# Performance work log

Hardware: AMD Instinct MI355X
Metric: run time of the kernel (lower is better)

The kernel has to match this reference:

```python
import jax, jax.numpy as jnp
import numpy as np

KERNEL_SIZES = (3, 5, 7)
NUM_HEAD = 6
DIM = 192
K_SCALES = 3
HEADS_PER_SCALE = NUM_HEAD // K_SCALES  # 2
HEAD_DIM = DIM // NUM_HEAD              # 32
SCALE = HEAD_DIM ** -0.5


def _nbr_idx(L, K):
    # NATTEN non-causal, dilation=1: window centered on query, clamped at edges.
    start = jnp.clip(jnp.arange(L) - K // 2, 0, L - K)
    return start[:, None] + jnp.arange(K)  # [L, K]


def _na3d_branch(xi, K):
    # xi: [B, D, H, W, C] with C = 3 * HEADS_PER_SCALE * HEAD_DIM
    B, D, H, W, C = xi.shape
    qkv = xi.reshape(B, D, H, W, 3, HEADS_PER_SCALE, HEAD_DIM).transpose(4, 0, 5, 1, 2, 3, 6)
    q, k, v = qkv[0] * SCALE, qkv[1], qkv[2]  # each [B, h, D, H, W, hd]

    idd, idh, idw = _nbr_idx(D, K), _nbr_idx(H, K), _nbr_idx(W, K)

    def gather(t):
        t = jnp.take(t, idd, axis=2)  # [B,h,D,K,H,W,hd]
        t = jnp.take(t, idh, axis=4)  # [B,h,D,K,H,K,W,hd]
        t = jnp.take(t, idw, axis=6)  # [B,h,D,K,H,K,W,K,hd]
        return t

    kn = gather(k)
    vn = gather(v)
    # attention logits over the K^3 neighborhood per query
    attn = jnp.einsum('bndhwc,bndihjwkc->bndhwijk', q, kn)
    attn = jax.nn.softmax(attn.reshape(B, HEADS_PER_SCALE, D, H, W, K ** 3), axis=-1)
    attn = attn.reshape(B, HEADS_PER_SCALE, D, H, W, K, K, K)
    y = jnp.einsum('bndhwijk,bndihjwkc->bndhwc', attn, vn)
    # [B,h,D,H,W,hd] -> [B,D,H,W,h*hd]
    return y.transpose(0, 2, 3, 4, 1, 5).reshape(B, D, H, W, HEADS_PER_SCALE * HEAD_DIM)


def setup_inputs() -> dict:
    key = jax.random.key(0)
    k0, k1, k2 = jax.random.split(key, 3)
    x = jax.random.normal(k0, (1, 8, 24, 24, DIM), dtype=jnp.float32)
    W_qkv = jax.random.normal(k1, (DIM, 3 * DIM), dtype=jnp.float32) * 0.02
    b_qkv = jnp.zeros((3 * DIM,), dtype=jnp.float32)
    W_proj = jax.random.normal(k2, (DIM, DIM), dtype=jnp.float32) * 0.02
    b_proj = jnp.zeros((DIM,), dtype=jnp.float32)
    return {'x': x, 'W_qkv': W_qkv, 'b_qkv': b_qkv, 'W_proj': W_proj, 'b_proj': b_proj}


def reference(x, W_qkv, b_qkv, W_proj, b_proj):
    qkv = x @ W_qkv + b_qkv  # [B,D,H,W,3*DIM]
    # torch.split with channels [DIM, DIM, DIM]
    chunks = jnp.split(qkv, K_SCALES, axis=4)
    ys = [_na3d_branch(chunks[i], KERNEL_SIZES[i]) for i in range(K_SCALES)]
    y = jnp.concatenate(ys, axis=4)  # [B,D,H,W,DIM]
    return y @ W_proj + b_proj
```

## Files before the change

### kernel.cpp

```cpp
#include <hip/hip_runtime.h>

typedef unsigned short ushort_t;
typedef unsigned int uint_t;
typedef __attribute__((ext_vector_type(8))) _Float16 half8;
typedef __attribute__((ext_vector_type(4))) float f32x4;

constexpr int DD = 8, HH = 24, WW = 24;
constexpr int NQ = DD * HH * WW;
constexpr int CIN = 192;
constexpr int CQKV = 576;
constexpr int KW = 192;
constexpr float SCALE_LOG2E = 0.17677669529663687f * 1.4426950408889634f;
constexpr int NROW = DD * HH;

__device__ __forceinline__ ushort_t bf16h(float x) {
    uint_t u = __float_as_uint(x);
    u += 0x7FFFu + ((u >> 16) & 1u);
    return (ushort_t)(u >> 16);
}
__device__ __forceinline__ float2 unpack2(uint_t u) {
    return make_float2(__uint_as_float(u << 16),
                       __uint_as_float(u & 0xffff0000u));
}
__device__ __forceinline__ ushort_t f16h(float x) {
    _Float16 h = (_Float16)x;
    return __builtin_bit_cast(ushort_t, h);
}
__device__ __forceinline__ float f16f(ushort_t h) {
    return (float)__builtin_bit_cast(_Float16, h);
}
__device__ __forceinline__ float quad_add_xor1(float x) {
    return x + __int_as_float(__builtin_amdgcn_mov_dpp(__float_as_int(x), 0xB1, 0xF, 0xF, true));
}
__device__ __forceinline__ float quad_add_xor2(float x) {
    return x + __int_as_float(__builtin_amdgcn_mov_dpp(__float_as_int(x), 0x4E, 0xF, 0xF, true));
}

constexpr int EB0 = 0;
constexpr int EB1 = NROW * 2 * WW * 2;
constexpr int EB2 = EB1 + NROW * 3 * WW * 2;
constexpr int ETOT = EB2 + NROW * 4 * WW * 2;

__global__ __launch_bounds__(256)
void convert_w_kernel(const float* __restrict__ Wq, const float* __restrict__ Wp,
                      ushort_t* __restrict__ Bq, ushort_t* __restrict__ Bp)
{
    __shared__ float T[32][36];
    int b = blockIdx.x;
    const float* W; ushort_t* Bb; int N;
    int kt, nt;
    if (b < 108) { W = Wq; Bb = Bq; N = CQKV; kt = b % 6; nt = b / 6; }
    else         { b -= 108; W = Wp; Bb = Bp; N = CIN; kt = b % 6; nt = b / 6; }
    const int k0 = kt * 32, n0 = nt * 32;
    const int tid = threadIdx.x;

    #pragma unroll
    for (int p = 0; p < 4; ++p) {
        int e = p * 256 + tid;
        int r = e >> 5, c = e & 31;
        T[c][r] = W[(long)(k0 + r) * N + n0 + c];
    }
    __syncthreads();
    const int n = tid >> 3;
    const int k4 = (tid & 7) * 4;
    float4 v = *(const float4*)(&T[n][k4]);
    ushort4 hv;
    hv.x = f16h(v.x); hv.y = f16h(v.y); hv.z = f16h(v.z); hv.w = f16h(v.w);
    *(ushort4*)(Bb + (long)(n0 + n) * KW + k0 + k4) = hv;
}

__global__ __launch_bounds__(256)
void gemm_mfma_kernel(const float* __restrict__ A, const ushort_t* __restrict__ Bb,
                      const float* __restrict__ bias, ushort_t* __restrict__ Cout, int N)
{
    __shared__ ushort_t As[64][72];
    __shared__ ushort_t Bs[64][72];
    __shared__ float Ct[64][68];

    const int tid = threadIdx.x;
    const int bm = blockIdx.x * 64;
    const int bn = blockIdx.y * 64;

    const int wv = tid >> 6;
    const int lane = tid & 63;
    const int lm = lane & 15;
    const int quad = lane >> 4;
    const int wr = (wv >> 1) * 32;
    const int wc = (wv & 1) * 32;

    const int ar = tid >> 4;
    const int ac4 = (tid & 15) * 4;
    const int br0 = tid >> 3;
    const int bc0 = (tid & 7) * 8;

    f32x4 acc[2][2] = {};

    float4 av[4];
    #pragma unroll
    for (int p = 0; p < 4; ++p)
        av[p] = *(const float4*)(A + (long)(bm + ar + p * 16) * CIN + ac4);
    uint4 nb0 = *(const uint4*)(Bb + (long)(bn + br0) * KW + bc0);
    uint4 nb1 = *(const uint4*)(Bb + (long)(bn + br0 + 32) * KW + bc0);

    #pragma unroll
    for (int g = 0; g < 3; ++g) {
        const uint4 b0 = nb0, b1 = nb1;
        ushort4 hv4[4], lv4[4];
        #pragma unroll
        for (int p = 0; p < 4; ++p) {
            float4 v = av[p];
            hv4[p].x = f16h(v.x); hv4[p].y = f16h(v.y);
            hv4[p].z = f16h(v.z); hv4[p].w = f16h(v.w);
            lv4[p].x = f16h(v.x - f16f(hv4[p].x));
            lv4[p].y = f16h(v.y - f16f(hv4[p].y));
            lv4[p].z = f16h(v.z - f16f(hv4[p].z));
            lv4[p].w = f16h(v.w - f16f(hv4[p].w));
        }
        __syncthreads();
        #pragma unroll
        for (int p = 0; p < 4; ++p)
            *(ushort4*)(&As[ar + p * 16][ac4]) = hv4[p];
        *(uint4*)(&Bs[br0][bc0])      = b0;
        *(uint4*)(&Bs[br0 + 32][bc0]) = b1;
        if (g < 2) {
            const int kk = (g + 1) * 64;
            nb0 = *(const uint4*)(Bb + (long)(bn + br0) * KW + kk + bc0);
            nb1 = *(const uint4*)(Bb + (long)(bn + br0 + 32) * KW + kk + bc0);
            #pragma unroll
            for (int p = 0; p < 4; ++p)
                av[p] = *(const float4*)(A + (long)(bm + ar + p * 16) * CIN + (g + 1) * 64 + ac4);
        }
        __syncthreads();

        #pragma unroll
        for (int ks = 0; ks < 64; ks += 32) {
            half8 af0 = *(const half8*)(&As[wr + lm][ks + quad * 8]);
            half8 af1 = *(const half8*)(&As[wr + 16 + lm][ks + quad * 8]);
            half8 bf0 = *(const half8*)(&Bs[wc + lm][ks + quad * 8]);
            half8 bf1 = *(const half8*)(&Bs[wc + 16 + lm][ks + quad * 8]);
            acc[0][0] = __builtin_amdgcn_mfma_f32_16x16x32_f16(af0, bf0, acc[0][0], 0, 0, 0);
            acc[0][1] = __builtin_amdgcn_mfma_f32_16x16x32_f16(af0, bf1, acc[0][1], 0, 0, 0);
            acc[1][0] = __builtin_amdgcn_mfma_f32_16x16x32_f16(af1, bf0, acc[1][0], 0, 0, 0);
            acc[1][1] = __builtin_amdgcn_mfma_f32_16x16x32_f16(af1, bf1, acc[1][1], 0, 0, 0);
        }
        __syncthreads();
        #pragma unroll
        for (int p = 0; p < 4; ++p)
            *(ushort4*)(&As[ar + p * 16][ac4]) = lv4[p];
        __syncthreads();
        #pragma unroll
        for (int ks = 0; ks < 64; ks += 32) {
            half8 af0 = *(const half8*)(&As[wr + lm][ks + quad * 8]);
            half8 af1 = *(const half8*)(&As[wr + 16 + lm][ks + quad * 8]);
            half8 bf0 = *(const half8*)(&Bs[wc + lm][ks + quad * 8]);
            half8 bf1 = *(const half8*)(&Bs[wc + 16 + lm][ks + quad * 8]);
            acc[0][0] = __builtin_amdgcn_mfma_f32_16x16x32_f16(af0, bf0, acc[0][0], 0, 0, 0);
            acc[0][1] = __builtin_amdgcn_mfma_f32_16x16x32_f16(af0, bf1, acc[0][1], 0, 0, 0);
            acc[1][0] = __builtin_amdgcn_mfma_f32_16x16x32_f16(af1, bf0, acc[1][0], 0, 0, 0);
            acc[1][1] = __builtin_amdgcn_mfma_f32_16x16x32_f16(af1, bf1, acc[1][1], 0, 0, 0);
        }
    }

    #pragma unroll
    for (int tc = 0; tc < 2; ++tc) {
        const float bv = bias[bn + wc + tc * 16 + lm];
        #pragma unroll
        for (int tr = 0; tr < 2; ++tr) {
            #pragma unroll
            for (int reg = 0; reg < 4; ++reg)
                Ct[wr + tr * 16 + quad * 4 + reg][wc + tc * 16 + lm] = acc[tr][tc][reg] + bv;
        }
    }
    __syncthreads();
    const int orow = tid >> 4;
    const int oc4 = (tid & 15) * 4;
    #pragma unroll
    for (int p = 0; p < 4; ++p) {
        const int r = orow + p * 16;
        float4 v = *(const float4*)(&Ct[r][oc4]);
        ushort4 hv;
        hv.x = bf16h(v.x); hv.y = bf16h(v.y); hv.z = bf16h(v.z); hv.w = bf16h(v.w);
        *(ushort4*)(Cout + (long)(bm + r) * N + bn + oc4) = hv;
    }
}

__global__ __launch_bounds__(256)
void gemm_proj_kernel(const float* __restrict__ accs, const float* __restrict__ stats,
                      const ushort_t* __restrict__ Bb, const float* __restrict__ bias,
                      float* __restrict__ Cout)
{
    __shared__ ushort_t As[64][72];
    __shared__ ushort_t Bs[64][72];
    __shared__ float Ct[64][68];

    const int tid = threadIdx.x;
    const int bm = blockIdx.x * 64;
    const int bn = blockIdx.y * 64;

    const int wv = tid >> 6;
    const int lane = tid & 63;
    const int lm = lane & 15;
    const int quad = lane >> 4;
    const int wr = (wv >> 1) * 32;
    const int wc = (wv & 1) * 32;

    const int ar = tid >> 4;
    const int ac4 = (tid & 15) * 4;
    const int a_hd = ac4 >> 5;
    const int a_cc = ac4 & 31;
    const int br0 = tid >> 3;
    const int bc0 = (tid & 7) * 8;

    f32x4 acc[2][2] = {};

    auto load_av = [&](int gg, float4* av) {
        const int CK = gg + 2;
        const int eb = (gg == 0) ? EB0 : (gg == 1 ? EB1 : EB2);
        #pragma unroll
        for (int p = 0; p < 4; ++p) {
            const int q = bm + ar + p * 16;
            const int rr = q / WW;
            const int w = q - rr * WW;
            const int e0 = eb + (rr * CK) * (WW * 2) + w * 2 + a_hd;
            float S = 0.f;
            float4 a = make_float4(0.f, 0.f, 0.f, 0.f);
            #pragma unroll
            for (int c = 0; c < 4; ++c) {
                if (c < CK) {
                    const int e = e0 + c * (WW * 2);
                    S += stats[e];
                    const float4 t = *(const float4*)(accs + (long)e * 32 + a_cc);
                    a.x += t.x; a.y += t.y; a.z += t.z; a.w += t.w;
                }
            }
            const float rs = 1.0f / S;
            av[p] = make_float4(a.x * rs, a.y * rs, a.z * rs, a.w * rs);
        }
    };

    float4 av[4];
    load_av(0, av);
    uint4 nb0 = *(const uint4*)(Bb + (long)(bn + br0) * KW + bc0);
    uint4 nb1 = *(const uint4*)(Bb + (long)(bn + br0 + 32) * KW + bc0);

    #pragma unroll
    for (int g = 0; g < 3; ++g) {
        const uint4 b0 = nb0, b1 = nb1;
        ushort4 hv4[4], lv4[4];
        #pragma unroll
        for (int p = 0; p < 4; ++p) {
            float4 v = av[p];
            hv4[p].x = f16h(v.x); hv4[p].y = f16h(v.y);
            hv4[p].z = f16h(v.z); hv4[p].w = f16h(v.w);
            lv4[p].x = f16h(v.x - f16f(hv4[p].x));
            lv4[p].y = f16h(v.y - f16f(hv4[p].y));
            lv4[p].z = f16h(v.z - f16f(hv4[p].z));
            lv4[p].w = f16h(v.w - f16f(hv4[p].w));
        }
        __syncthreads();
        #pragma unroll
        for (int p = 0; p < 4; ++p)
            *(ushort4*)(&As[ar + p * 16][ac4]) = hv4[p];
        *(uint4*)(&Bs[br0][bc0])      = b0;
        *(uint4*)(&Bs[br0 + 32][bc0]) = b1;
        if (g < 2) {
            const int kk = (g + 1) * 64;
            nb0 = *(const uint4*)(Bb + (long)(bn + br0) * KW + kk + bc0);
            nb1 = *(const uint4*)(Bb + (long)(bn + br0 + 32) * KW + kk + bc0);
            load_av(g + 1, av);
        }
        __syncthreads();

        #pragma unroll
        for (int ks = 0; ks < 64; ks += 32) {
            half8 af0 = *(const half8*)(&As[wr + lm][ks + quad * 8]);
            half8 af1 = *(const half8*)(&As[wr + 16 + lm][ks + quad * 8]);
            half8 bf0 = *(const half8*)(&Bs[wc + lm][ks + quad * 8]);
            half8 bf1 = *(const half8*)(&Bs[wc + 16 + lm][ks + quad * 8]);
            acc[0][0] = __builtin_amdgcn_mfma_f32_16x16x32_f16(af0, bf0, acc[0][0], 0, 0, 0);
            acc[0][1] = __builtin_amdgcn_mfma_f32_16x16x32_f16(af0, bf1, acc[0][1], 0, 0, 0);
            acc[1][0] = __builtin_amdgcn_mfma_f32_16x16x32_f16(af1, bf0, acc[1][0], 0, 0, 0);
            acc[1][1] = __builtin_amdgcn_mfma_f32_16x16x32_f16(af1, bf1, acc[1][1], 0, 0, 0);
        }
        __syncthreads();
        #pragma unroll
        for (int p = 0; p < 4; ++p)
            *(ushort4*)(&As[ar + p * 16][ac4]) = lv4[p];
        __syncthreads();
        #pragma unroll
        for (int ks = 0; ks < 64; ks += 32) {
            half8 af0 = *(const half8*)(&As[wr + lm][ks + quad * 8]);
            half8 af1 = *(const half8*)(&As[wr + 16 + lm][ks + quad * 8]);
            half8 bf0 = *(const half8*)(&Bs[wc + lm][ks + quad * 8]);
            half8 bf1 = *(const half8*)(&Bs[wc + 16 + lm][ks + quad * 8]);
            acc[0][0] = __builtin_amdgcn_mfma_f32_16x16x32_f16(af0, bf0, acc[0][0], 0, 0, 0);
            acc[0][1] = __builtin_amdgcn_mfma_f32_16x16x32_f16(af0, bf1, acc[0][1], 0, 0, 0);
            acc[1][0] = __builtin_amdgcn_mfma_f32_16x16x32_f16(af1, bf0, acc[1][0], 0, 0, 0);
            acc[1][1] = __builtin_amdgcn_mfma_f32_16x16x32_f16(af1, bf1, acc[1][1], 0, 0, 0);
        }
    }

    #pragma unroll
    for (int tc = 0; tc < 2; ++tc) {
        const float bv = bias[bn + wc + tc * 16 + lm];
        #pragma unroll
        for (int tr = 0; tr < 2; ++tr) {
            #pragma unroll
            for (int reg = 0; reg < 4; ++reg)
                Ct[wr + tr * 16 + quad * 4 + reg][wc + tc * 16 + lm] = acc[tr][tc][reg] + bv;
        }
    }
    __syncthreads();
    const int orow = tid >> 4;
    const int oc4 = (tid & 15) * 4;
    #pragma unroll
    for (int p = 0; p < 4; ++p) {
        const int r = orow + p * 16;
        float4 v = *(const float4*)(&Ct[r][oc4]);
        *(float4*)(Cout + (long)(bm + r) * CIN + bn + oc4) = v;
    }
}

constexpr int KROW = 72;
constexpr int RBUF = WW * KROW;

template<int K>
__device__ __forceinline__
void split_chunk(const ushort_t* __restrict__ qkv,
                 float* __restrict__ accs, float* __restrict__ stats,
                 int r, int c, int nchunks, int scale, int ebase,
                 int w, int hd, int d8, int tid,
                 ushort_t* __restrict__ ksh, ushort_t* __restrict__ vsh)
{
    const int i0 = 2 * c;
    const int ni = (K - i0) < 2 ? (K - i0) : 2;
    const int NT = ni * K;

    const int dq = r / HH, hq = r % HH;
    int sd = dq - K / 2; sd = sd < 0 ? 0 : (sd > DD - K ? DD - K : sd);
    int sh = hq - K / 2; sh = sh < 0 ? 0 : (sh > HH - K ? HH - K : sh);
    int sw = w  - K / 2; sw = sw < 0 ? 0 : (sw > WW - K ? WW - K : sw);

    const int q = (dq * HH + hq) * WW + w;

    uint4 qu = *(const uint4*)(qkv + (long)q * CQKV + scale * 192 + hd * 32 + d8 * 8);
    float2 qf[4] = {unpack2(qu.x), unpack2(qu.y), unpack2(qu.z), unpack2(qu.w)};
    #pragma unroll
    for (int t = 0; t < 4; ++t) {
        qf[t].x *= SCALE_LOG2E;
        qf[t].y *= SCALE_LOG2E;
    }

    const int lw = tid >> 3;
    const int c8 = (tid & 7) * 8;

    auto src_ptr = [&](int t) {
        int i = i0 + t / K;
        int j = t - (t / K) * K;
        return qkv + (long)(((sd + i) * HH + (sh + j)) * WW + lw) * CQKV
             + scale * 192 + c8;
    };

    uint4 ck, cv;
    {
        const ushort_t* p0 = src_ptr(0);
        uint4 k0 = *(const uint4*)(p0 + 64);
        uint4 v0 = *(const uint4*)(p0 + 128);
        const ushort_t* p1 = src_ptr(1);
        ck = *(const uint4*)(p1 + 64);
        cv = *(const uint4*)(p1 + 128);
        *(uint4*)(ksh + lw * KROW + c8) = k0;
        *(uint4*)(vsh + lw * KROW + c8) = v0;
    }

    float sum = 0.f;
    float2 acc[4] = {};
    const int choff = hd * 32 + d8 * 8;

    for (int t = 0; t < NT; ++t) {
        __syncthreads();
        uint4 nk, nv;
        const bool issue = (t + 2 < NT);
        if (issue) {
            const ushort_t* pn = src_ptr(t + 2);
            nk = *(const uint4*)(pn + 64);
            nv = *(const uint4*)(pn + 128);
        }

        const ushort_t* kb = ksh + (t % 3) * RBUF + choff;
        const ushort_t* vb = vsh + (t % 3) * RBUF + choff;
        #pragma unroll
        for (int n = 0; n < K; ++n) {
            uint4 ku = *(const uint4*)(kb + (sw + n) * KROW);
            float2 k0 = unpack2(ku.x), k1 = unpack2(ku.y),
                   k2 = unpack2(ku.z), k3 = unpack2(ku.w);
            float2 d;
            d.x  = qf[0].x * k0.x; d.y  = qf[0].y * k0.y;
            d.x += qf[1].x * k1.x; d.y += qf[1].y * k1.y;
            d.x += qf[2].x * k2.x; d.y += qf[2].y * k2.y;
            d.x += qf[3].x * k3.x; d.y += qf[3].y * k3.y;
            float p = d.x + d.y;
            p = quad_add_xor1(p);
            p = quad_add_xor2(p);
            float pr = exp2f(p);
            sum += pr;
            uint4 vu = *(const uint4*)(vb + (sw + n) * KROW);
            float2 v0 = unpack2(vu.x), v1 = unpack2(vu.y),
                   v2 = unpack2(vu.z), v3 = unpack2(vu.w);
            acc[0].x += pr * v0.x; acc[0].y += pr * v0.y;
            acc[1].x += pr * v1.x; acc[1].y += pr * v1.y;
            acc[2].x += pr * v2.x; acc[2].y += pr * v2.y;
            acc[3].x += pr * v3.x; acc[3].y += pr * v3.y;
        }

        if (t + 1 < NT) {
            *(uint4*)(ksh + ((t + 1) % 3) * RBUF + lw * KROW + c8) = ck;
            *(uint4*)(vsh + ((t + 1) % 3) * RBUF + lw * KROW + c8) = cv;
        }
        ck = nk; cv = nv;
    }

    const int e = ebase + ((r * nchunks + c) * WW + w) * 2 + hd;
    if (d8 == 0) stats[e] = sum;
    float* ap = accs + (long)e * 32 + d8 * 8;
    *(float4*)(ap)     = make_float4(acc[0].x, acc[0].y, acc[1].x, acc[1].y);
    *(float4*)(ap + 4) = make_float4(acc[2].x, acc[2].y, acc[3].x, acc[3].y);
}

__global__ __launch_bounds__(192)
void na3d_split_kernel(const ushort_t* __restrict__ qkv,
                       float* __restrict__ accs, float* __restrict__ stats)
{
    __shared__ alignas(16) ushort_t ksh[3 * RBUF];
    __shared__ alignas(16) ushort_t vsh[3 * RBUF];

    const int tid = threadIdx.x;
    const int w  = tid >> 3;
    const int hd = (tid >> 2) & 1;
    const int d8 = tid & 3;

    const int orig = blockIdx.x;
    int bid;
    if (orig < NROW * 4) {
        bid = (orig & 7) * (NROW * 4 / 8) + (orig >> 3);
    } else if (orig < NROW * 7) {
        const int t = orig - NROW * 4;
        bid = NROW * 4 + (t & 7) * (NROW * 3 / 8) + (t >> 3);
    } else {
        const int t = orig - NROW * 7;
        bid = NROW * 7 + (t & 7) * (NROW * 2 / 8) + (t >> 3);
    }

    if (bid < NROW * 4) {
        int r = bid >> 2, c = bid & 3;
        split_chunk<7>(qkv, accs, stats, r, c, 4, 2, EB2, w, hd, d8, tid, ksh, vsh);
    } else if (bid < NROW * 4 + NROW * 3) {
        int t = bid - NROW * 4;
        int r = t / 3, c = t - (t / 3) * 3;
        split_chunk<5>(qkv, accs, stats, r, c, 3, 1, EB1, w, hd, d8, tid, ksh, vsh);
    } else {
        int t = bid - NROW * 7;
        int r = t >> 1, c = t & 1;
        split_chunk<3>(qkv, accs, stats, r, c, 2, 0, EB0, w, hd, d8, tid, ksh, vsh);
    }
}

extern "C" void kernel_launch(void* const* d_in, const int* in_sizes, int n_in,
                              void* d_out, int out_size, void* d_ws, size_t ws_size,
                              hipStream_t stream)
{
    const float* x      = (const float*)d_in[0];
    const float* W_qkv  = (const float*)d_in[1];
    const float* b_qkv  = (const float*)d_in[2];
    const float* W_proj = (const float*)d_in[3];
    const float* b_proj = (const float*)d_in[4];
    float* out = (float*)d_out;

    float* accs    = (float*)d_ws;
    float* stats   = accs + (long)ETOT * 32;
    ushort_t* qkvb = (ushort_t*)(stats + ETOT);
    ushort_t* Wbq  = qkvb + (long)NQ * CQKV;
    ushort_t* Wbp  = Wbq + (long)CQKV * KW;

    convert_w_kernel<<<dim3(144), 256, 0, stream>>>(W_qkv, W_proj, Wbq, Wbp);

    gemm_mfma_kernel<<<dim3(NQ / 64, CQKV / 64), 256, 0, stream>>>(x, Wbq, b_qkv, qkvb, CQKV);

    na3d_split_kernel<<<dim3(NROW * (4 + 3 + 2)), 192, 0, stream>>>(qkvb, accs, stats);

    gemm_proj_kernel<<<dim3(NQ / 64, CIN / 64), 256, 0, stream>>>(accs, stats, Wbp, b_proj, out);
}
```

Baseline: 106.9 us.

## Process two query rows per block and two adjacent queries per thread

Each block of the neighborhood-attention split kernel now covers two (d,h) rows, one per half of its threads, and each thread handles two adjacent w positions. Both queries share a single scan over the K+1 key/value columns, with masking for the columns outside each window. This halves the block count and reuses each LDS load of K and V across two queries to cut shared-memory traffic per query. In exchange the kernel uses twice the LDS, more registers per thread, and does one extra masked column of work per step.

```diff
diff --git a/kernel.cpp b/kernel.cpp
--- a/kernel.cpp
+++ b/kernel.cpp
@@ -322,16 +322,23 @@
 }
 
 constexpr int KROW = 72;
-constexpr int RBUF = WW * KROW;
+constexpr int RT = 24 * KROW;
 
 template<int K>
 __device__ __forceinline__
 void split_chunk(const ushort_t* __restrict__ qkv,
                  float* __restrict__ accs, float* __restrict__ stats,
-                 int r, int c, int nchunks, int scale, int ebase,
-                 int w, int hd, int d8, int tid,
-                 ushort_t* __restrict__ ksh, ushort_t* __restrict__ vsh)
+                 int r0, int c, int nchunks, int scale, int ebase,
+                 int tid, ushort_t* __restrict__ ksh, ushort_t* __restrict__ vsh)
 {
+    const int rhalf = tid >= 96 ? 1 : 0;
+    const int t96 = tid - rhalf * 96;
+    const int slot = t96 >> 3;
+    const int hd = (t96 >> 2) & 1;
+    const int d8 = t96 & 3;
+    const int w0 = slot * 2, w1 = w0 + 1;
+    const int r = r0 + rhalf;
+
     const int i0 = 2 * c;
     const int ni = (K - i0) < 2 ? (K - i0) : 2;
     const int NT = ni * K;
@@ -339,129 +346,166 @@
     const int dq = r / HH, hq = r % HH;
     int sd = dq - K / 2; sd = sd < 0 ? 0 : (sd > DD - K ? DD - K : sd);
     int sh = hq - K / 2; sh = sh < 0 ? 0 : (sh > HH - K ? HH - K : sh);
-    int sw = w  - K / 2; sw = sw < 0 ? 0 : (sw > WW - K ? WW - K : sw);
-
-    const int q = (dq * HH + hq) * WW + w;
-
-    uint4 qu = *(const uint4*)(qkv + (long)q * CQKV + scale * 192 + hd * 32 + d8 * 8);
-    float2 qf[4] = {unpack2(qu.x), unpack2(qu.y), unpack2(qu.z), unpack2(qu.w)};
+    int sw0 = w0 - K / 2; sw0 = sw0 < 0 ? 0 : (sw0 > WW - K ? WW - K : sw0);
+    int sw1 = w1 - K / 2; sw1 = sw1 < 0 ? 0 : (sw1 > WW - K ? WW - K : sw1);
+
+    const long qbase = (long)((dq * HH + hq) * WW) * CQKV + scale * 192 + hd * 32 + d8 * 8;
+    uint4 qu0 = *(const uint4*)(qkv + qbase + (long)w0 * CQKV);
+    uint4 qu1 = *(const uint4*)(qkv + qbase + (long)w1 * CQKV);
+    float2 qf0[4] = {unpack2(qu0.x), unpack2(qu0.y), unpack2(qu0.z), unpack2(qu0.w)};
+    float2 qf1[4] = {unpack2(qu1.x), unpack2(qu1.y), unpack2(qu1.z), unpack2(qu1.w)};
     #pragma unroll
     for (int t = 0; t < 4; ++t) {
-        qf[t].x *= SCALE_LOG2E;
-        qf[t].y *= SCALE_LOG2E;
-    }
-
-    const int lw = tid >> 3;
-    const int c8 = (tid & 7) * 8;
+        qf0[t].x *= SCALE_LOG2E; qf0[t].y *= SCALE_LOG2E;
+        qf1[t].x *= SCALE_LOG2E; qf1[t].y *= SCALE_LOG2E;
+    }
+
+    const int sr = t96 >> 2;
+    const int sc = (t96 & 3) * 16;
 
     auto src_ptr = [&](int t) {
         int i = i0 + t / K;
         int j = t - (t / K) * K;
-        return qkv + (long)(((sd + i) * HH + (sh + j)) * WW + lw) * CQKV
-             + scale * 192 + c8;
+        return qkv + (long)(((sd + i) * HH + (sh + j)) * WW + sr) * CQKV
+             + scale * 192 + sc;
     };
-
-    uint4 ck, cv;
+    auto lds_off = [&](int buf) {
+        return (buf * 2 + rhalf) * RT + sr * KROW + sc;
+    };
+
+    uint4 ck0, ck1, cv0, cv1;
     {
         const ushort_t* p0 = src_ptr(0);
-        uint4 k0 = *(const uint4*)(p0 + 64);
-        uint4 v0 = *(const uint4*)(p0 + 128);
+        uint4 k0a = *(const uint4*)(p0 + 64);
+        uint4 k0b = *(const uint4*)(p0 + 72);
+        uint4 v0a = *(const uint4*)(p0 + 128);
+        uint4 v0b = *(const uint4*)(p0 + 136);
         const ushort_t* p1 = src_ptr(1);
-        ck = *(const uint4*)(p1 + 64);
-        cv = *(const uint4*)(p1 + 128);
-        *(uint4*)(ksh + lw * KROW + c8) = k0;
-        *(uint4*)(vsh + lw * KROW + c8) = v0;
-    }
-
-    float sum = 0.f;
-    float2 acc[4] = {};
+        ck0 = *(const uint4*)(p1 + 64);
+        ck1 = *(const uint4*)(p1 + 72);
+        cv0 = *(const uint4*)(p1 + 128);
+        cv1 = *(const uint4*)(p1 + 136);
+        const int lb = lds_off(0);
+        *(uint4*)(ksh + lb)     = k0a;
+        *(uint4*)(ksh + lb + 8) = k0b;
+        *(uint4*)(vsh + lb)     = v0a;
+        *(uint4*)(vsh + lb + 8) = v0b;
+    }
+
+    float sum0 = 0.f, sum1 = 0.f;
+    float2 a0[4] = {}, a1[4] = {};
     const int choff = hd * 32 + d8 * 8;
 
     for (int t = 0; t < NT; ++t) {
         __syncthreads();
-        uint4 nk, nv;
+        uint4 nk0, nk1, nv0, nv1;
         const bool issue = (t + 2 < NT);
         if (issue) {
             const ushort_t* pn = src_ptr(t + 2);
-            nk = *(const uint4*)(pn + 64);
-            nv = *(const uint4*)(pn + 128);
-        }
-
-        const ushort_t* kb = ksh + (t % 3) * RBUF + choff;
-        const ushort_t* vb = vsh + (t % 3) * RBUF + choff;
-        #pragma unroll
-        for (int n = 0; n < K; ++n) {
-            uint4 ku = *(const uint4*)(kb + (sw + n) * KROW);
+            nk0 = *(const uint4*)(pn + 64);
+            nk1 = *(const uint4*)(pn + 72);
+            nv0 = *(const uint4*)(pn + 128);
+            nv1 = *(const uint4*)(pn + 136);
+        }
+
+        const int bb = ((t % 3) * 2 + rhalf) * RT + choff;
+        #pragma unroll
+        for (int n = 0; n <= K; ++n) {
+            const int row = sw0 + n;
+            const int rowc = row < WW ? row : WW - 1;
+            const bool m0 = (n < K);
+            const bool m1 = (row >= sw1) && (row < sw1 + K);
+            uint4 ku = *(const uint4*)(ksh + bb + rowc * KROW);
             float2 k0 = unpack2(ku.x), k1 = unpack2(ku.y),
                    k2 = unpack2(ku.z), k3 = unpack2(ku.w);
-            float2 d;
-            d.x  = qf[0].x * k0.x; d.y  = qf[0].y * k0.y;
-            d.x += qf[1].x * k1.x; d.y += qf[1].y * k1.y;
-            d.x += qf[2].x * k2.x; d.y += qf[2].y * k2.y;
-            d.x += qf[3].x * k3.x; d.y += qf[3].y * k3.y;
-            float p = d.x + d.y;
-            p = quad_add_xor1(p);
-            p = quad_add_xor2(p);
-            float pr = exp2f(p);
-            sum += pr;
-            uint4 vu = *(const uint4*)(vb + (sw + n) * KROW);
+            float2 d0, d1;
+            d0.x  = qf0[0].x * k0.x; d0.y  = qf0[0].y * k0.y;
+            d0.x += qf0[1].x * k1.x; d0.y += qf0[1].y * k1.y;
+            d0.x += qf0[2].x * k2.x; d0.y += qf0[2].y * k2.y;
+            d0.x += qf0[3].x * k3.x; d0.y += qf0[3].y * k3.y;
+            d1.x  = qf1[0].x * k0.x; d1.y  = qf1[0].y * k0.y;
+            d1.x += qf1[1].x * k1.x; d1.y += qf1[1].y * k1.y;
+            d1.x += qf1[2].x * k2.x; d1.y += qf1[2].y * k2.y;
+            d1.x += qf1[3].x * k3.x; d1.y += qf1[3].y * k3.y;
+            float p0 = d0.x + d0.y;
+            p0 = quad_add_xor1(p0);
+            p0 = quad_add_xor2(p0);
+            float p1 = d1.x + d1.y;
+            p1 = quad_add_xor1(p1);
+            p1 = quad_add_xor2(p1);
+            float pr0 = m0 ? exp2f(p0) : 0.f;
+            float pr1 = m1 ? exp2f(p1) : 0.f;
+            sum0 += pr0;
+            sum1 += pr1;
+            uint4 vu = *(const uint4*)(vsh + bb + rowc * KROW);
             float2 v0 = unpack2(vu.x), v1 = unpack2(vu.y),
                    v2 = unpack2(vu.z), v3 = unpack2(vu.w);
-            acc[0].x += pr * v0.x; acc[0].y += pr * v0.y;
-            acc[1].x += pr * v1.x; acc[1].y += pr * v1.y;
-            acc[2].x += pr * v2.x; acc[2].y += pr * v2.y;
-            acc[3].x += pr * v3.x; acc[3].y += pr * v3.y;
+            a0[0].x += pr0 * v0.x; a0[0].y += pr0 * v0.y;
+            a0[1].x += pr0 * v1.x; a0[1].y += pr0 * v1.y;
+            a0[2].x += pr0 * v2.x; a0[2].y += pr0 * v2.y;
+            a0[3].x += pr0 * v3.x; a0[3].y += pr0 * v3.y;
+            a1[0].x += pr1 * v0.x; a1[0].y += pr1 * v0.y;
+            a1[1].x += pr1 * v1.x; a1[1].y += pr1 * v1.y;
+            a1[2].x += pr1 * v2.x; a1[2].y += pr1 * v2.y;
+            a1[3].x += pr1 * v3.x; a1[3].y += pr1 * v3.y;
         }
 
         if (t + 1 < NT) {
-            *(uint4*)(ksh + ((t + 1) % 3) * RBUF + lw * KROW + c8) = ck;
-            *(uint4*)(vsh + ((t + 1) % 3) * RBUF + lw * KROW + c8) = cv;
-        }
-        ck = nk; cv = nv;
-    }
-
-    const int e = ebase + ((r * nchunks + c) * WW + w) * 2 + hd;
-    if (d8 == 0) stats[e] = sum;
-    float* ap = accs + (long)e * 32 + d8 * 8;
-    *(float4*)(ap)     = make_float4(acc[0].x, acc[0].y, acc[1].x, acc[1].y);
-    *(float4*)(ap + 4) = make_float4(acc[2].x, acc[2].y, acc[3].x, acc[3].y);
+            const int lb = lds_off((t + 1) % 3);
+            *(uint4*)(ksh + lb)     = ck0;
+            *(uint4*)(ksh + lb + 8) = ck1;
+            *(uint4*)(vsh + lb)     = cv0;
+            *(uint4*)(vsh + lb + 8) = cv1;
+        }
+        ck0 = nk0; ck1 = nk1; cv0 = nv0; cv1 = nv1;
+    }
+
+    const int e0 = ebase + ((r * nchunks + c) * WW + w0) * 2 + hd;
+    const int e1 = e0 + 2;
+    if (d8 == 0) {
+        stats[e0] = sum0;
+        stats[e1] = sum1;
+    }
+    float* ap0 = accs + (long)e0 * 32 + d8 * 8;
+    *(float4*)(ap0)     = make_float4(a0[0].x, a0[0].y, a0[1].x, a0[1].y);
+    *(float4*)(ap0 + 4) = make_float4(a0[2].x, a0[2].y, a0[3].x, a0[3].y);
+    float* ap1 = accs + (long)e1 * 32 + d8 * 8;
+    *(float4*)(ap1)     = make_float4(a1[0].x, a1[0].y, a1[1].x, a1[1].y);
+    *(float4*)(ap1 + 4) = make_float4(a1[2].x, a1[2].y, a1[3].x, a1[3].y);
 }
 
 __global__ __launch_bounds__(192)
 void na3d_split_kernel(const ushort_t* __restrict__ qkv,
                        float* __restrict__ accs, float* __restrict__ stats)
 {
-    __shared__ alignas(16) ushort_t ksh[3 * RBUF];
-    __shared__ alignas(16) ushort_t vsh[3 * RBUF];
+    __shared__ alignas(16) ushort_t ksh[3 * 2 * RT];
+    __shared__ alignas(16) ushort_t vsh[3 * 2 * RT];
 
     const int tid = threadIdx.x;
-    const int w  = tid >> 3;
-    const int hd = (tid >> 2) & 1;
-    const int d8 = tid & 3;
 
     const int orig = blockIdx.x;
     int bid;
-    if (orig < NROW * 4) {
-        bid = (orig & 7) * (NROW * 4 / 8) + (orig >> 3);
-    } else if (orig < NROW * 7) {
-        const int t = orig - NROW * 4;
-        bid = NROW * 4 + (t & 7) * (NROW * 3 / 8) + (t >> 3);
+    if (orig < 384) {
+        bid = (orig & 7) * 48 + (orig >> 3);
+    } else if (orig < 672) {
+        const int t = orig - 384;
+        bid = 384 + (t & 7) * 36 + (t >> 3);
     } else {
-        const int t = orig - NROW * 7;
-        bid = NROW * 7 + (t & 7) * (NROW * 2 / 8) + (t >> 3);
-    }
-
-    if (bid < NROW * 4) {
-        int r = bid >> 2, c = bid & 3;
-        split_chunk<7>(qkv, accs, stats, r, c, 4, 2, EB2, w, hd, d8, tid, ksh, vsh);
-    } else if (bid < NROW * 4 + NROW * 3) {
-        int t = bid - NROW * 4;
-        int r = t / 3, c = t - (t / 3) * 3;
-        split_chunk<5>(qkv, accs, stats, r, c, 3, 1, EB1, w, hd, d8, tid, ksh, vsh);
+        const int t = orig - 672;
+        bid = 672 + (t & 7) * 24 + (t >> 3);
+    }
+
+    if (bid < 384) {
+        int rp = bid >> 2, c = bid & 3;
+        split_chunk<7>(qkv, accs, stats, rp * 2, c, 4, 2, EB2, tid, ksh, vsh);
+    } else if (bid < 672) {
+        int t = bid - 384;
+        int rp = t / 3, c = t - (t / 3) * 3;
+        split_chunk<5>(qkv, accs, stats, rp * 2, c, 3, 1, EB1, tid, ksh, vsh);
     } else {
-        int t = bid - NROW * 7;
-        int r = t >> 1, c = t & 1;
-        split_chunk<3>(qkv, accs, stats, r, c, 2, 0, EB0, w, hd, d8, tid, ksh, vsh);
+        int t = bid - 672;
+        int rp = t >> 1, c = t & 1;
+        split_chunk<3>(qkv, accs, stats, rp * 2, c, 2, 0, EB0, tid, ksh, vsh);
     }
 }
 
@@ -486,7 +530,7 @@
 
     gemm_mfma_kernel<<<dim3(NQ / 64, CQKV / 64), 256, 0, stream>>>(x, Wbq, b_qkv, qkvb, CQKV);
 
-    na3d_split_kernel<<<dim3(NROW * (4 + 3 + 2)), 192, 0, stream>>>(qkvb, accs, stats);
+    na3d_split_kernel<<<dim3(384 + 288 + 192), 192, 0, stream>>>(qkvb, accs, stats);
 
     gemm_proj_kernel<<<dim3(NQ / 64, CIN / 64), 256, 0, stream>>>(accs, stats, Wbp, b_proj, out);
 }
```

Measured after the change: 115.4 us. +7.9%, slower.

## Replace block-wide barriers with per-wave private K/V staging in split kernel

Applied to the files above, without the earlier changes.

Each of the three waves now loads the full 24-row K/V plane into its own private LDS slice, single-buffered. The block-wide __syncthreads in the neighbor loop is replaced by wave-local lgkmcnt waits. This removes inter-wave barrier stalls across the K*ni planes. In exchange it triples global/L2 load traffic and LDS writes per block, and prefetch depth drops from two planes ahead to one.

```diff
diff --git a/kernel.cpp b/kernel.cpp
--- a/kernel.cpp
+++ b/kernel.cpp
@@ -322,16 +322,24 @@
 }
 
 constexpr int KROW = 72;
-constexpr int RBUF = WW * KROW;
+constexpr int RT = 24 * KROW;
 
 template<int K>
 __device__ __forceinline__
 void split_chunk(const ushort_t* __restrict__ qkv,
                  float* __restrict__ accs, float* __restrict__ stats,
                  int r, int c, int nchunks, int scale, int ebase,
-                 int w, int hd, int d8, int tid,
-                 ushort_t* __restrict__ ksh, ushort_t* __restrict__ vsh)
+                 int tid, ushort_t* __restrict__ ksh, ushort_t* __restrict__ vsh)
 {
+    const int wave = tid >> 6;
+    const int lane = tid & 63;
+    const int w  = tid >> 3;
+    const int hd = (lane >> 2) & 1;
+    const int d8 = lane & 3;
+
+    ushort_t* kb = ksh + wave * RT;
+    ushort_t* vb = vsh + wave * RT;
+
     const int i0 = 2 * c;
     const int ni = (K - i0) < 2 ? (K - i0) : 2;
     const int NT = ni * K;
@@ -351,26 +359,39 @@
         qf[t].y *= SCALE_LOG2E;
     }
 
-    const int lw = tid >> 3;
-    const int c8 = (tid & 7) * 8;
-
-    auto src_ptr = [&](int t) {
+    auto src_plane = [&](int t) {
         int i = i0 + t / K;
         int j = t - (t / K) * K;
-        return qkv + (long)(((sd + i) * HH + (sh + j)) * WW + lw) * CQKV
-             + scale * 192 + c8;
+        return qkv + (long)(((sd + i) * HH + (sh + j)) * WW) * CQKV + scale * 192;
     };
 
-    uint4 ck, cv;
+    uint4 ck[3], cv[3];
+
     {
-        const ushort_t* p0 = src_ptr(0);
-        uint4 k0 = *(const uint4*)(p0 + 64);
-        uint4 v0 = *(const uint4*)(p0 + 128);
-        const ushort_t* p1 = src_ptr(1);
-        ck = *(const uint4*)(p1 + 64);
-        cv = *(const uint4*)(p1 + 128);
-        *(uint4*)(ksh + lw * KROW + c8) = k0;
-        *(uint4*)(vsh + lw * KROW + c8) = v0;
+        const ushort_t* p0 = src_plane(0);
+        uint4 tk[3], tv[3];
+        #pragma unroll
+        for (int m = 0; m < 3; ++m) {
+            const int e = lane + 64 * m;
+            const int sr = e >> 3, sc = (e & 7) * 8;
+            tk[m] = *(const uint4*)(p0 + (long)sr * CQKV + 64 + sc);
+            tv[m] = *(const uint4*)(p0 + (long)sr * CQKV + 128 + sc);
+        }
+        const ushort_t* p1 = src_plane(1);
+        #pragma unroll
+        for (int m = 0; m < 3; ++m) {
+            const int e = lane + 64 * m;
+            const int sr = e >> 3, sc = (e & 7) * 8;
+            ck[m] = *(const uint4*)(p1 + (long)sr * CQKV + 64 + sc);
+            cv[m] = *(const uint4*)(p1 + (long)sr * CQKV + 128 + sc);
+        }
+        #pragma unroll
+        for (int m = 0; m < 3; ++m) {
+            const int e = lane + 64 * m;
+            const int sr = e >> 3, sc = (e & 7) * 8;
+            *(uint4*)(kb + sr * KROW + sc) = tk[m];
+            *(uint4*)(vb + sr * KROW + sc) = tv[m];
+        }
     }
 
     float sum = 0.f;
@@ -378,20 +399,11 @@
     const int choff = hd * 32 + d8 * 8;
 
     for (int t = 0; t < NT; ++t) {
-        __syncthreads();
-        uint4 nk, nv;
-        const bool issue = (t + 2 < NT);
-        if (issue) {
-            const ushort_t* pn = src_ptr(t + 2);
-            nk = *(const uint4*)(pn + 64);
-            nv = *(const uint4*)(pn + 128);
-        }
-
-        const ushort_t* kb = ksh + (t % 3) * RBUF + choff;
-        const ushort_t* vb = vsh + (t % 3) * RBUF + choff;
+        asm volatile("s_waitcnt lgkmcnt(0)" ::: "memory");
+
         #pragma unroll
         for (int n = 0; n < K; ++n) {
-            uint4 ku = *(const uint4*)(kb + (sw + n) * KROW);
+            uint4 ku = *(const uint4*)(kb + (sw + n) * KROW + choff);
             float2 k0 = unpack2(ku.x), k1 = unpack2(ku.y),
                    k2 = unpack2(ku.z), k3 = unpack2(ku.w);
             float2 d;
@@ -404,7 +416,7 @@
             p = quad_add_xor2(p);
             float pr = exp2f(p);
             sum += pr;
-            uint4 vu = *(const uint4*)(vb + (sw + n) * KROW);
+            uint4 vu = *(const uint4*)(vb + (sw + n) * KROW + choff);
             float2 v0 = unpack2(vu.x), v1 = unpack2(vu.y),
                    v2 = unpack2(vu.z), v3 = unpack2(vu.w);
             acc[0].x += pr * v0.x; acc[0].y += pr * v0.y;
@@ -414,10 +426,25 @@
         }
 
         if (t + 1 < NT) {
-            *(uint4*)(ksh + ((t + 1) % 3) * RBUF + lw * KROW + c8) = ck;
-            *(uint4*)(vsh + ((t + 1) % 3) * RBUF + lw * KROW + c8) = cv;
-        }
-        ck = nk; cv = nv;
+            asm volatile("s_waitcnt lgkmcnt(0)" ::: "memory");
+            #pragma unroll
+            for (int m = 0; m < 3; ++m) {
+                const int e = lane + 64 * m;
+                const int sr = e >> 3, sc = (e & 7) * 8;
+                *(uint4*)(kb + sr * KROW + sc) = ck[m];
+                *(uint4*)(vb + sr * KROW + sc) = cv[m];
+            }
+            if (t + 2 < NT) {
+                const ushort_t* pn = src_plane(t + 2);
+                #pragma unroll
+                for (int m = 0; m < 3; ++m) {
+                    const int e = lane + 64 * m;
+                    const int sr = e >> 3, sc = (e & 7) * 8;
+                    ck[m] = *(const uint4*)(pn + (long)sr * CQKV + 64 + sc);
+                    cv[m] = *(const uint4*)(pn + (long)sr * CQKV + 128 + sc);
+                }
+            }
+        }
     }
 
     const int e = ebase + ((r * nchunks + c) * WW + w) * 2 + hd;
@@ -431,13 +458,10 @@
 void na3d_split_kernel(const ushort_t* __restrict__ qkv,
                        float* __restrict__ accs, float* __restrict__ stats)
 {
-    __shared__ alignas(16) ushort_t ksh[3 * RBUF];
-    __shared__ alignas(16) ushort_t vsh[3 * RBUF];
+    __shared__ alignas(16) ushort_t ksh[3 * RT];
+    __shared__ alignas(16) ushort_t vsh[3 * RT];
 
     const int tid = threadIdx.x;
-    const int w  = tid >> 3;
-    const int hd = (tid >> 2) & 1;
-    const int d8 = tid & 3;
 
     const int orig = blockIdx.x;
     int bid;
@@ -453,15 +477,15 @@
 
     if (bid < NROW * 4) {
         int r = bid >> 2, c = bid & 3;
-        split_chunk<7>(qkv, accs, stats, r, c, 4, 2, EB2, w, hd, d8, tid, ksh, vsh);
+        split_chunk<7>(qkv, accs, stats, r, c, 4, 2, EB2, tid, ksh, vsh);
     } else if (bid < NROW * 4 + NROW * 3) {
         int t = bid - NROW * 4;
         int r = t / 3, c = t - (t / 3) * 3;
-        split_chunk<5>(qkv, accs, stats, r, c, 3, 1, EB1, w, hd, d8, tid, ksh, vsh);
+        split_chunk<5>(qkv, accs, stats, r, c, 3, 1, EB1, tid, ksh, vsh);
     } else {
         int t = bid - NROW * 7;
         int r = t >> 1, c = t & 1;
-        split_chunk<3>(qkv, accs, stats, r, c, 2, 0, EB0, w, hd, d8, tid, ksh, vsh);
+        split_chunk<3>(qkv, accs, stats, r, c, 2, 0, EB0, tid, ksh, vsh);
     }
 }
 
```

Result: slower. 164.4 us (+53.8%).

## Read neighborhood K/V directly from global memory instead of LDS triple buffer

Applied to the files above, without the earlier changes.

Removes the shared-memory triple-buffered staging of key/value rows and the per-step block barrier in the neighborhood attention split kernel. Each thread now loads its K and V vectors for every neighbor straight from global memory (through the caches). This removes the barriers, LDS traffic and shared-memory footprint, which may raise occupancy. The cost is more redundant global/L2 reads, since neighboring queries in a block re-read overlapping windows and lose the explicit prefetch.

```diff
diff --git a/kernel.cpp b/kernel.cpp
--- a/kernel.cpp
+++ b/kernel.cpp
@@ -321,17 +321,16 @@
     }
 }
 
-constexpr int KROW = 72;
-constexpr int RBUF = WW * KROW;
-
 template<int K>
 __device__ __forceinline__
 void split_chunk(const ushort_t* __restrict__ qkv,
                  float* __restrict__ accs, float* __restrict__ stats,
-                 int r, int c, int nchunks, int scale, int ebase,
-                 int w, int hd, int d8, int tid,
-                 ushort_t* __restrict__ ksh, ushort_t* __restrict__ vsh)
-{
+                 int r, int c, int nchunks, int scale, int ebase, int tid)
+{
+    const int w  = tid >> 3;
+    const int hd = (tid >> 2) & 1;
+    const int d8 = tid & 3;
+
     const int i0 = 2 * c;
     const int ni = (K - i0) < 2 ? (K - i0) : 2;
     const int NT = ni * K;
@@ -351,47 +350,20 @@
         qf[t].y *= SCALE_LOG2E;
     }
 
-    const int lw = tid >> 3;
-    const int c8 = (tid & 7) * 8;
-
-    auto src_ptr = [&](int t) {
-        int i = i0 + t / K;
-        int j = t - (t / K) * K;
-        return qkv + (long)(((sd + i) * HH + (sh + j)) * WW + lw) * CQKV
-             + scale * 192 + c8;
-    };
-
-    uint4 ck, cv;
-    {
-        const ushort_t* p0 = src_ptr(0);
-        uint4 k0 = *(const uint4*)(p0 + 64);
-        uint4 v0 = *(const uint4*)(p0 + 128);
-        const ushort_t* p1 = src_ptr(1);
-        ck = *(const uint4*)(p1 + 64);
-        cv = *(const uint4*)(p1 + 128);
-        *(uint4*)(ksh + lw * KROW + c8) = k0;
-        *(uint4*)(vsh + lw * KROW + c8) = v0;
-    }
+    const int choff = 64 + hd * 32 + d8 * 8;
 
     float sum = 0.f;
     float2 acc[4] = {};
-    const int choff = hd * 32 + d8 * 8;
 
     for (int t = 0; t < NT; ++t) {
-        __syncthreads();
-        uint4 nk, nv;
-        const bool issue = (t + 2 < NT);
-        if (issue) {
-            const ushort_t* pn = src_ptr(t + 2);
-            nk = *(const uint4*)(pn + 64);
-            nv = *(const uint4*)(pn + 128);
-        }
-
-        const ushort_t* kb = ksh + (t % 3) * RBUF + choff;
-        const ushort_t* vb = vsh + (t % 3) * RBUF + choff;
+        const int i = i0 + t / K;
+        const int j = t - (t / K) * K;
+        const ushort_t* pl = qkv
+            + (long)(((sd + i) * HH + (sh + j)) * WW + sw) * CQKV
+            + scale * 192 + choff;
         #pragma unroll
         for (int n = 0; n < K; ++n) {
-            uint4 ku = *(const uint4*)(kb + (sw + n) * KROW);
+            uint4 ku = *(const uint4*)(pl + (long)n * CQKV);
             float2 k0 = unpack2(ku.x), k1 = unpack2(ku.y),
                    k2 = unpack2(ku.z), k3 = unpack2(ku.w);
             float2 d;
@@ -404,7 +376,7 @@
             p = quad_add_xor2(p);
             float pr = exp2f(p);
             sum += pr;
-            uint4 vu = *(const uint4*)(vb + (sw + n) * KROW);
+            uint4 vu = *(const uint4*)(pl + (long)n * CQKV + 64);
             float2 v0 = unpack2(vu.x), v1 = unpack2(vu.y),
                    v2 = unpack2(vu.z), v3 = unpack2(vu.w);
             acc[0].x += pr * v0.x; acc[0].y += pr * v0.y;
@@ -412,12 +384,6 @@
             acc[2].x += pr * v2.x; acc[2].y += pr * v2.y;
             acc[3].x += pr * v3.x; acc[3].y += pr * v3.y;
         }
-
-        if (t + 1 < NT) {
-            *(uint4*)(ksh + ((t + 1) % 3) * RBUF + lw * KROW + c8) = ck;
-            *(uint4*)(vsh + ((t + 1) % 3) * RBUF + lw * KROW + c8) = cv;
-        }
-        ck = nk; cv = nv;
     }
 
     const int e = ebase + ((r * nchunks + c) * WW + w) * 2 + hd;
@@ -431,13 +397,7 @@
 void na3d_split_kernel(const ushort_t* __restrict__ qkv,
                        float* __restrict__ accs, float* __restrict__ stats)
 {
-    __shared__ alignas(16) ushort_t ksh[3 * RBUF];
-    __shared__ alignas(16) ushort_t vsh[3 * RBUF];
-
     const int tid = threadIdx.x;
-    const int w  = tid >> 3;
-    const int hd = (tid >> 2) & 1;
-    const int d8 = tid & 3;
 
     const int orig = blockIdx.x;
     int bid;
@@ -453,15 +413,15 @@
 
     if (bid < NROW * 4) {
         int r = bid >> 2, c = bid & 3;
-        split_chunk<7>(qkv, accs, stats, r, c, 4, 2, EB2, w, hd, d8, tid, ksh, vsh);
+        split_chunk<7>(qkv, accs, stats, r, c, 4, 2, EB2, tid);
     } else if (bid < NROW * 4 + NROW * 3) {
         int t = bid - NROW * 4;
         int r = t / 3, c = t - (t / 3) * 3;
-        split_chunk<5>(qkv, accs, stats, r, c, 3, 1, EB1, w, hd, d8, tid, ksh, vsh);
+        split_chunk<5>(qkv, accs, stats, r, c, 3, 1, EB1, tid);
     } else {
         int t = bid - NROW * 7;
         int r = t >> 1, c = t & 1;
-        split_chunk<3>(qkv, accs, stats, r, c, 2, 0, EB0, w, hd, d8, tid, ksh, vsh);
+        split_chunk<3>(qkv, accs, stats, r, c, 2, 0, EB0, tid);
     }
 }
 
```

Result: slower. 121.7 us (+13.8%).
